# Optimization experiments

Measured on AMD Instinct MI355X. Metric: run time of the kernel, lower is better.

The kernel has to match this reference:

```python
import jax, jax.numpy as jnp
import numpy as np

DIM = 1024
HEADS = 16
HEAD_DIM = DIM // HEADS
SCALE = HEAD_DIM ** -0.5


def setup_inputs() -> dict:
    key = jax.random.key(0)
    k_x, k_win, k_wout, k_bout = jax.random.split(key, 4)
    x = jax.random.normal(k_x, (4, 2048, DIM), dtype=jnp.float32)
    # torch Linear: y = x @ W.T + b; store weights as [in, out] for jnp
    w_in = jax.random.normal(k_win, (DIM, 3 * DIM), dtype=jnp.float32) * (DIM ** -0.5)
    w_out = jax.random.normal(k_wout, (DIM, DIM), dtype=jnp.float32) * (DIM ** -0.5)
    b_out = jax.random.normal(k_bout, (DIM,), dtype=jnp.float32) * 0.02
    return {"x": x, "w_in": w_in, "w_out": w_out, "b_out": b_out}


def reference(x, w_in, w_out, b_out):
    b, n, _ = x.shape
    qkv = x @ w_in  # [b, n, 3*dim]
    q, k, v = jnp.split(qkv, 3, axis=-1)
    # [b, n, h*d] -> [b, h, n, d]
    def split_heads(t):
        return t.reshape(b, n, HEADS, HEAD_DIM).transpose(0, 2, 1, 3)
    q, k, v = split_heads(q), split_heads(k), split_heads(v)
    scores = jnp.einsum('bhid,bhjd->bhij', q, k) * SCALE
    attn = jax.nn.softmax(scores, axis=-1)  # dropout_rate=0 -> identity
    o = jnp.einsum('bhij,bhjd->bhid', attn, v)
    o = o.transpose(0, 2, 1, 3).reshape(b, n, HEADS * HEAD_DIM)
    return o @ w_out + b_out
```

## Files before the change

### kernel.cpp

```cpp
#include <hip/hip_runtime.h>

typedef unsigned short u16;
typedef __bf16 bf16x8 __attribute__((ext_vector_type(8)));
typedef float f32x4 __attribute__((ext_vector_type(4)));
typedef unsigned short u16x4 __attribute__((ext_vector_type(4)));
typedef unsigned short u16x8 __attribute__((ext_vector_type(8)));

#define DIM 1024
#define HEADS 16
#define HD 64
#define SEQ 2048
#define BATCH 4
#define NROWS (BATCH*SEQ)
#define C2 0.18033688f
#define THR_PS 1.125899907e15f

__device__ __forceinline__ u16 f2bf(float f) {
  union { float f; unsigned u; } v; v.f = f;
  unsigned r = v.u + 0x7FFFu + ((v.u >> 16) & 1u);
  return (u16)(r >> 16);
}

__device__ __forceinline__ unsigned cvt_pk_bf16(float lo, float hi) {
  unsigned r;
  asm("v_cvt_pk_bf16_f32 %0, %1, %2" : "=v"(r) : "v"(lo), "v"(hi));
  return r;
}

__device__ __forceinline__ f32x4 mfma16(bf16x8 a, bf16x8 b, f32x4 c) {
  return __builtin_amdgcn_mfma_f32_16x16x32_bf16(a, b, c, 0, 0, 0);
}

__device__ __forceinline__ void gl_lds16(const void* g, void* l) {
  __builtin_amdgcn_global_load_lds(
      (const __attribute__((address_space(1))) void*)g,
      (__attribute__((address_space(3))) void*)l, 16, 0, 0);
}

__global__ __launch_bounds__(256) void cast_f32_bf16(const float* __restrict__ in,
                                                     u16* __restrict__ out) {
  int i = blockIdx.x * 256 + threadIdx.x;
  float4 v = ((const float4*)in)[i];
  u16x4 o = { f2bf(v.x), f2bf(v.y), f2bf(v.z), f2bf(v.w) };
  *(u16x4*)(out + (size_t)i * 4) = o;
}

__global__ __launch_bounds__(256) void transpose_cast(const float* __restrict__ in,
                                                      u16* __restrict__ out,
                                                      int R, int C) {
  __shared__ u16 tile[64][65];
  int c0 = blockIdx.x * 64, r0 = blockIdx.y * 64;
  int tid = threadIdx.x;
#pragma unroll
  for (int i = 0; i < 16; ++i) {
    int idx = tid + i * 256;
    int r = idx >> 6, c = idx & 63;
    tile[c][r] = f2bf(in[(size_t)(r0 + r) * C + c0 + c]);
  }
  __syncthreads();
#pragma unroll
  for (int i = 0; i < 16; ++i) {
    int idx = tid + i * 256;
    int r = idx >> 6, c = idx & 63;
    out[(size_t)(c0 + r) * R + r0 + c] = tile[r][c];
  }
}

__global__ __launch_bounds__(256) void transpose_v(const u16* __restrict__ qkv,
                                                   u16* __restrict__ vT) {
  __shared__ unsigned t32[64][37];
  const int t = blockIdx.x, bh = blockIdx.y;
  const int b = bh >> 4, h = bh & 15;
  const u16* src = qkv + ((size_t)(b * SEQ + t * 64)) * 3072 + 2048 + h * 64;
  const int tid = threadIdx.x;
#pragma unroll
  for (int i = 0; i < 8; ++i) {
    int lin = tid + i * 256;
    int r2 = lin >> 6, c = lin & 63;
    unsigned lo = src[(size_t)(2 * r2) * 3072 + c];
    unsigned hi = src[(size_t)(2 * r2 + 1) * 3072 + c];
    t32[c][r2] = lo | (hi << 16);
  }
  __syncthreads();
  unsigned* dst = (unsigned*)(vT + (size_t)bh * 64 * 2048);
#pragma unroll
  for (int i = 0; i < 8; ++i) {
    int lin = tid + i * 256;
    int d = lin >> 5, r2 = lin & 31;
    int rp = (r2 & 16) | ((r2 & 6) << 1) | ((r2 & 8) >> 2) | (r2 & 1);
    dst[(size_t)d * 1024 + t * 32 + rp] = t32[d][r2];
  }
}

template<int OUT_F32>
__global__ __launch_bounds__(256) void gemm_bt(const u16* __restrict__ A,
                                               const u16* __restrict__ BT,
                                               void* __restrict__ Cout,
                                               const float* __restrict__ bias,
                                               int M, int N, int K) {
  __shared__ __align__(16) u16 As[128 * 64];
  __shared__ __align__(16) u16 Bs[128 * 64];
  const int tid = threadIdx.x;
  const int l = tid & 63, w = tid >> 6, g = l >> 4, ln = l & 15;
  const int m0 = blockIdx.y * 128, n0 = blockIdx.x * 128;
  const int wr = w >> 1, wc = w & 1;
  f32x4 acc[4][4];
#pragma unroll
  for (int i = 0; i < 4; ++i)
#pragma unroll
    for (int j = 0; j < 4; ++j) acc[i][j] = (f32x4){0.f, 0.f, 0.f, 0.f};

  const int srow = tid >> 3;
  const int scol = (tid & 7) * 8;
  const u16* Asrc = A  + (size_t)(m0 + srow) * K + scol;
  const u16* Bsrc = BT + (size_t)(n0 + srow) * K + scol;
  char* AsB = (char*)As + (size_t)w * 1024;
  char* BsB = (char*)Bs + (size_t)w * 1024;

  const int nk = K >> 6;
  for (int kt = 0; kt < nk; ++kt) {
    const u16* a0 = Asrc + kt * 64;
    const u16* b0 = Bsrc + kt * 64;
#pragma unroll
    for (int is = 0; is < 4; ++is) {
      gl_lds16(a0 + (size_t)is * 32 * K, AsB + is * 4096);
      gl_lds16(b0 + (size_t)is * 32 * K, BsB + is * 4096);
    }
    __syncthreads();
#pragma unroll
    for (int kk = 0; kk < 2; ++kk) {
      bf16x8 af[4], bfr[4];
#pragma unroll
      for (int i = 0; i < 4; ++i) {
        af[i]  = *(const bf16x8*)(As + (wr * 64 + i * 16 + ln) * 64 + kk * 32 + g * 8);
        bfr[i] = *(const bf16x8*)(Bs + (wc * 64 + i * 16 + ln) * 64 + kk * 32 + g * 8);
      }
#pragma unroll
      for (int mi = 0; mi < 4; ++mi)
#pragma unroll
        for (int ni = 0; ni < 4; ++ni)
          acc[mi][ni] = mfma16(af[mi], bfr[ni], acc[mi][ni]);
    }
    __syncthreads();
  }
#pragma unroll
  for (int mi = 0; mi < 4; ++mi) {
#pragma unroll
    for (int ni = 0; ni < 4; ++ni) {
      int col = n0 + wc * 64 + ni * 16 + ln;
#pragma unroll
      for (int j = 0; j < 4; ++j) {
        int row = m0 + wr * 64 + mi * 16 + g * 4 + j;
        float v = acc[mi][ni][j];
        if (OUT_F32) {
          ((float*)Cout)[(size_t)row * N + col] = v + bias[col];
        } else {
          ((u16*)Cout)[(size_t)row * N + col] = f2bf(v);
        }
      }
    }
  }
}

__global__ __launch_bounds__(256) void attn_kernel(const u16* __restrict__ qkv,
                                                   const u16* __restrict__ vT,
                                                   u16* __restrict__ obuf) {
  __shared__ __align__(16) u16 k_lds[2][64 * 64];
  __shared__ __align__(16) u16 v_lds[2][64 * 64];
  const int wg = blockIdx.x;
  const int j = (wg & 7) * 128 + (wg >> 3);
  const int qt = j & 15, h = (j >> 4) & 15, b = j >> 8;
  const int tid = threadIdx.x;
  const int w = tid >> 6, l = tid & 63, g = l >> 4, ln = l & 15;
  const int qbase = qt * 128 + w * 32;
  const size_t rs = 3 * DIM;

  bf16x8 qf[2][2];
#pragma unroll
  for (int e = 0; e < 2; ++e) {
    const u16* qb = qkv + (size_t)(b * SEQ + qbase + e * 16 + ln) * rs + h * HD;
    qf[e][0] = *(const bf16x8*)(qb + g * 8);
    qf[e][1] = *(const bf16x8*)(qb + 32 + g * 8);
  }

  const int krow = tid >> 3;
  const int ksrccol = ((((tid & 7) << 4) ^ ((krow & 7) << 4))) >> 1;
  const u16* kbase = qkv + (size_t)b * SEQ * rs + DIM + h * HD;
  const u16* vtb = vT + (size_t)(b * HEADS + h) * 64 * 2048;
  const int swz = (ln & 7) << 4;

  float m[2] = { -1e30f, -1e30f }, lsum[2] = { 0.f, 0.f };
  f32x4 of[2][4];
#pragma unroll
  for (int e = 0; e < 2; ++e)
#pragma unroll
    for (int i = 0; i < 4; ++i) of[e][i] = (f32x4){0.f, 0.f, 0.f, 0.f};

  auto stage = [&](int buf, int kv0) {
    const u16* ks0 = kbase + (size_t)(kv0 + krow) * rs + ksrccol;
    const u16* vs0 = vtb + (size_t)krow * 2048 + kv0 + ksrccol;
    char* kd = (char*)(&k_lds[buf][0]) + (size_t)w * 1024;
    char* vd = (char*)(&v_lds[buf][0]) + (size_t)w * 1024;
    gl_lds16(ks0, kd);
    gl_lds16(ks0 + (size_t)32 * rs, kd + 4096);
    gl_lds16(vs0, vd);
    gl_lds16(vs0 + (size_t)32 * 2048, vd + 4096);
  };

  stage(0, 0);
  __syncthreads();
  int cur = 0;

  for (int t = 0; t < 32; ++t) {
    if (t < 31) stage(cur ^ 1, (t + 1) * 64);

    f32x4 sacc[2][4];
#pragma unroll
    for (int e = 0; e < 2; ++e)
#pragma unroll
      for (int f = 0; f < 4; ++f) sacc[e][f] = (f32x4){0.f, 0.f, 0.f, 0.f};
#pragma unroll
    for (int f = 0; f < 4; ++f) {
      const char* kr = (const char*)(&k_lds[cur][0]) + (f * 16 + ln) * 128;
      bf16x8 a0 = *(const bf16x8*)(kr + ((g * 16) ^ swz));
      bf16x8 a1 = *(const bf16x8*)(kr + ((64 | (g * 16)) ^ swz));
#pragma unroll
      for (int e = 0; e < 2; ++e) {
        sacc[e][f] = mfma16(a0, qf[e][0], sacc[e][f]);
        sacc[e][f] = mfma16(a1, qf[e][1], sacc[e][f]);
      }
    }

    union pu { unsigned wd[4]; bf16x8 bv; } pf[2][2];
    float ps[2];
#pragma unroll
    for (int e = 0; e < 2; ++e) {
      const float mc = m[e] * C2;
      float s2 = 0.f;
#pragma unroll
      for (int f = 0; f < 4; ++f)
#pragma unroll
        for (int j2 = 0; j2 < 2; ++j2) {
          float p0 = __builtin_amdgcn_exp2f(fmaf(sacc[e][f][2 * j2], C2, -mc));
          float p1 = __builtin_amdgcn_exp2f(fmaf(sacc[e][f][2 * j2 + 1], C2, -mc));
          s2 += p0 + p1;
          pf[e][f >> 1].wd[(f & 1) * 2 + j2] = cvt_pk_bf16(p0, p1);
        }
      s2 += __shfl_xor(s2, 16);
      s2 += __shfl_xor(s2, 32);
      ps[e] = s2;
    }
    if (__any(fmaxf(ps[0], ps[1]) > THR_PS)) {
#pragma unroll
      for (int e = 0; e < 2; ++e) {
        float tm = -3e38f;
#pragma unroll
        for (int f = 0; f < 4; ++f)
#pragma unroll
          for (int jj = 0; jj < 4; ++jj) tm = fmaxf(tm, sacc[e][f][jj]);
        tm = fmaxf(tm, __shfl_xor(tm, 16));
        tm = fmaxf(tm, __shfl_xor(tm, 32));
        float mn = fmaxf(m[e], tm);
        float rc = __builtin_amdgcn_exp2f((m[e] - mn) * C2);
        lsum[e] *= rc;
#pragma unroll
        for (int fd = 0; fd < 4; ++fd) of[e][fd] *= rc;
        m[e] = mn;
        const float mc = mn * C2;
        float s2 = 0.f;
#pragma unroll
        for (int f = 0; f < 4; ++f)
#pragma unroll
          for (int j2 = 0; j2 < 2; ++j2) {
            float p0 = __builtin_amdgcn_exp2f(fmaf(sacc[e][f][2 * j2], C2, -mc));
            float p1 = __builtin_amdgcn_exp2f(fmaf(sacc[e][f][2 * j2 + 1], C2, -mc));
            s2 += p0 + p1;
            pf[e][f >> 1].wd[(f & 1) * 2 + j2] = cvt_pk_bf16(p0, p1);
          }
        s2 += __shfl_xor(s2, 16);
        s2 += __shfl_xor(s2, 32);
        ps[e] = s2;
      }
    }
    lsum[0] += ps[0];
    lsum[1] += ps[1];

#pragma unroll
    for (int kk = 0; kk < 2; ++kk)
#pragma unroll
      for (int fd = 0; fd < 4; ++fd) {
        const char* vr = (const char*)(&v_lds[cur][0]) + (fd * 16 + ln) * 128;
        bf16x8 fa = *(const bf16x8*)(vr + ((kk * 64 + g * 16) ^ swz));
#pragma unroll
        for (int e = 0; e < 2; ++e)
          of[e][fd] = mfma16(fa, pf[e][kk].bv, of[e][fd]);
      }

    __syncthreads();
    cur ^= 1;
  }

#pragma unroll
  for (int e = 0; e < 2; ++e) {
    float linv = 1.f / lsum[e];
    u16* orow = obuf + (size_t)(b * SEQ + qbase + e * 16 + ln) * DIM + h * HD;
#pragma unroll
    for (int fd = 0; fd < 4; ++fd) {
      unsigned w0 = cvt_pk_bf16(of[e][fd][0] * linv, of[e][fd][1] * linv);
      unsigned w1 = cvt_pk_bf16(of[e][fd][2] * linv, of[e][fd][3] * linv);
      unsigned* dst = (unsigned*)(orow + fd * 16 + g * 4);
      dst[0] = w0;
      dst[1] = w1;
    }
  }
}

extern "C" void kernel_launch(void* const* d_in, const int* in_sizes, int n_in,
                              void* d_out, int out_size, void* d_ws, size_t ws_size,
                              hipStream_t stream) {
  const float* x     = (const float*)d_in[0];
  const float* w_in  = (const float*)d_in[1];
  const float* w_out = (const float*)d_in[2];
  const float* b_out = (const float*)d_in[3];
  float* out = (float*)d_out;

  char* ws = (char*)d_ws;
  u16* xb     = (u16*)(ws);
  u16* vT     = (u16*)(ws);
  u16* w_inT  = (u16*)(ws + (size_t)16 * 1024 * 1024);
  u16* w_outT = (u16*)(ws + (size_t)22 * 1024 * 1024);
  u16* qkv    = (u16*)(ws + (size_t)24 * 1024 * 1024);
  u16* obuf   = (u16*)(ws + (size_t)72 * 1024 * 1024);

  cast_f32_bf16<<<8192, 256, 0, stream>>>(x, xb);
  transpose_cast<<<dim3(48, 16), 256, 0, stream>>>(w_in, w_inT, 1024, 3072);
  transpose_cast<<<dim3(16, 16), 256, 0, stream>>>(w_out, w_outT, 1024, 1024);
  gemm_bt<0><<<dim3(24, 64), 256, 0, stream>>>(xb, w_inT, qkv, nullptr, NROWS, 3 * DIM, DIM);
  transpose_v<<<dim3(32, 64), 256, 0, stream>>>(qkv, vT);
  attn_kernel<<<1024, 256, 0, stream>>>(qkv, vT, obuf);
  gemm_bt<1><<<dim3(8, 64), 256, 0, stream>>>(obuf, w_outT, out, b_out, NROWS, DIM, DIM);
}
```

Measured before the change: 233.4 us.

## Remap GEMM tiles per XCD, add MFMA priority hints, defer softmax row-sum reduction

The GEMM launches switch to a 1D grid that remaps block ids so that consecutive tiles land on the same XCD, which is meant to improve L2 reuse across the eight chiplets. The attention kernel wraps its MFMA sections in s_setprio so matrix work gets issue priority over the softmax code of other waves. The per-iteration cross-lane shuffles for the row sum are removed, and partial sums are accumulated per lane and reduced once at the end. The overflow-rescale check now tests partial sums rather than full ones, which slightly changes when rescaling triggers.

```diff
diff --git a/kernel.cpp b/kernel.cpp
--- a/kernel.cpp
+++ b/kernel.cpp
@@ -97,12 +97,14 @@
                                                const u16* __restrict__ BT,
                                                void* __restrict__ Cout,
                                                const float* __restrict__ bias,
-                                               int M, int N, int K) {
+                                               int M, int N, int K, int nx) {
   __shared__ __align__(16) u16 As[128 * 64];
   __shared__ __align__(16) u16 Bs[128 * 64];
   const int tid = threadIdx.x;
   const int l = tid & 63, w = tid >> 6, g = l >> 4, ln = l & 15;
-  const int m0 = blockIdx.y * 128, n0 = blockIdx.x * 128;
+  const int cpx = gridDim.x >> 3;
+  const int jj = (blockIdx.x & 7) * cpx + (blockIdx.x >> 3);
+  const int n0 = (jj % nx) * 128, m0 = (jj / nx) * 128;
   const int wr = w >> 1, wc = w & 1;
   f32x4 acc[4][4];
 #pragma unroll
@@ -189,7 +191,7 @@
   const u16* vtb = vT + (size_t)(b * HEADS + h) * 64 * 2048;
   const int swz = (ln & 7) << 4;
 
-  float m[2] = { -1e30f, -1e30f }, lsum[2] = { 0.f, 0.f };
+  float m[2] = { -1e30f, -1e30f }, psac[2] = { 0.f, 0.f };
   f32x4 of[2][4];
 #pragma unroll
   for (int e = 0; e < 2; ++e)
@@ -219,6 +221,7 @@
     for (int e = 0; e < 2; ++e)
 #pragma unroll
       for (int f = 0; f < 4; ++f) sacc[e][f] = (f32x4){0.f, 0.f, 0.f, 0.f};
+    __builtin_amdgcn_s_setprio(1);
 #pragma unroll
     for (int f = 0; f < 4; ++f) {
       const char* kr = (const char*)(&k_lds[cur][0]) + (f * 16 + ln) * 128;
@@ -230,6 +233,7 @@
         sacc[e][f] = mfma16(a1, qf[e][1], sacc[e][f]);
       }
     }
+    __builtin_amdgcn_s_setprio(0);
 
     union pu { unsigned wd[4]; bf16x8 bv; } pf[2][2];
     float ps[2];
@@ -246,8 +250,6 @@
           s2 += p0 + p1;
           pf[e][f >> 1].wd[(f & 1) * 2 + j2] = cvt_pk_bf16(p0, p1);
         }
-      s2 += __shfl_xor(s2, 16);
-      s2 += __shfl_xor(s2, 32);
       ps[e] = s2;
     }
     if (__any(fmaxf(ps[0], ps[1]) > THR_PS)) {
@@ -262,7 +264,7 @@
         tm = fmaxf(tm, __shfl_xor(tm, 32));
         float mn = fmaxf(m[e], tm);
         float rc = __builtin_amdgcn_exp2f((m[e] - mn) * C2);
-        lsum[e] *= rc;
+        psac[e] *= rc;
 #pragma unroll
         for (int fd = 0; fd < 4; ++fd) of[e][fd] *= rc;
         m[e] = mn;
@@ -277,14 +279,13 @@
             s2 += p0 + p1;
             pf[e][f >> 1].wd[(f & 1) * 2 + j2] = cvt_pk_bf16(p0, p1);
           }
-        s2 += __shfl_xor(s2, 16);
-        s2 += __shfl_xor(s2, 32);
         ps[e] = s2;
       }
     }
-    lsum[0] += ps[0];
-    lsum[1] += ps[1];
-
+    psac[0] += ps[0];
+    psac[1] += ps[1];
+
+    __builtin_amdgcn_s_setprio(1);
 #pragma unroll
     for (int kk = 0; kk < 2; ++kk)
 #pragma unroll
@@ -295,6 +296,7 @@
         for (int e = 0; e < 2; ++e)
           of[e][fd] = mfma16(fa, pf[e][kk].bv, of[e][fd]);
       }
+    __builtin_amdgcn_s_setprio(0);
 
     __syncthreads();
     cur ^= 1;
@@ -302,7 +304,10 @@
 
 #pragma unroll
   for (int e = 0; e < 2; ++e) {
-    float linv = 1.f / lsum[e];
+    float ls = psac[e];
+    ls += __shfl_xor(ls, 16);
+    ls += __shfl_xor(ls, 32);
+    float linv = 1.f / ls;
     u16* orow = obuf + (size_t)(b * SEQ + qbase + e * 16 + ln) * DIM + h * HD;
 #pragma unroll
     for (int fd = 0; fd < 4; ++fd) {
@@ -335,8 +340,8 @@
   cast_f32_bf16<<<8192, 256, 0, stream>>>(x, xb);
   transpose_cast<<<dim3(48, 16), 256, 0, stream>>>(w_in, w_inT, 1024, 3072);
   transpose_cast<<<dim3(16, 16), 256, 0, stream>>>(w_out, w_outT, 1024, 1024);
-  gemm_bt<0><<<dim3(24, 64), 256, 0, stream>>>(xb, w_inT, qkv, nullptr, NROWS, 3 * DIM, DIM);
+  gemm_bt<0><<<1536, 256, 0, stream>>>(xb, w_inT, qkv, nullptr, NROWS, 3 * DIM, DIM, 24);
   transpose_v<<<dim3(32, 64), 256, 0, stream>>>(qkv, vT);
   attn_kernel<<<1024, 256, 0, stream>>>(qkv, vT, obuf);
-  gemm_bt<1><<<dim3(8, 64), 256, 0, stream>>>(obuf, w_outT, out, b_out, NROWS, DIM, DIM);
-}
+  gemm_bt<1><<<512, 256, 0, stream>>>(obuf, w_outT, out, b_out, NROWS, DIM, DIM, 8);
+}
```

Result: no change. 234.5 us (+0.5%).
